# Kernel tuning notes

Hardware: AMD Instinct MI355X
Metric: run time of the kernel (lower is better)

## Reference

```python
import jax, jax.numpy as jnp
import numpy as np

LN_EPS = 1e-5

def _layernorm(x, g, b):
    mu = jnp.mean(x, axis=-1, keepdims=True)
    var = jnp.var(x, axis=-1, keepdims=True)
    return (x - mu) * jax.lax.rsqrt(var + LN_EPS) * g + b

def setup_inputs() -> dict:
    key = jax.random.key(0)
    B, S, D, H = 2, 2048, 1024, 16
    dh = D // H          # 64
    r = 48               # r_attn = int(0.75*min(D,dh))
    r_out = 768          # int(0.75*D)
    I = 4 * D            # GPT-2 MLP inner dim
    r_mlp = 512          # int(0.5*min(D,I))
    ks = jax.random.split(key, 24)
    sc = lambda *sh: 0.02
    inp = {
        'hidden_states': jax.random.normal(ks[0], (B, S, D), jnp.float32),
        'ln1_g': jnp.ones((D,), jnp.float32), 'ln1_b': jnp.zeros((D,), jnp.float32),
        'ln2_g': jnp.ones((D,), jnp.float32), 'ln2_b': jnp.zeros((D,), jnp.float32),
        'q_U': jax.random.normal(ks[1], (D, H, r), jnp.float32) * 0.02,
        'q_V': jax.random.normal(ks[2], (H, r, dh), jnp.float32) * 0.02,
        'q_b': jax.random.normal(ks[3], (H, dh), jnp.float32) * 0.02,
        'k_U': jax.random.normal(ks[4], (D, H, r), jnp.float32) * 0.02,
        'k_V': jax.random.normal(ks[5], (H, r, dh), jnp.float32) * 0.02,
        'k_b': jax.random.normal(ks[6], (H, dh), jnp.float32) * 0.02,
        'v_U': jax.random.normal(ks[7], (D, H, r), jnp.float32) * 0.02,
        'v_V': jax.random.normal(ks[8], (H, r, dh), jnp.float32) * 0.02,
        'v_b': jax.random.normal(ks[9], (H, dh), jnp.float32) * 0.02,
        'out_U': jax.random.normal(ks[10], (D, r_out), jnp.float32) * 0.02,
        'out_V': jax.random.normal(ks[11], (r_out, D), jnp.float32) * 0.02,
        'out_b': jnp.zeros((D,), jnp.float32),
        'fc1_U': jax.random.normal(ks[12], (D, r_mlp), jnp.float32) * 0.02,
        'fc1_V': jax.random.normal(ks[13], (r_mlp, I), jnp.float32) * 0.02,
        'fc1_b': jnp.zeros((I,), jnp.float32),
        'fc2_U': jax.random.normal(ks[14], (I, r_mlp), jnp.float32) * 0.02,
        'fc2_V': jax.random.normal(ks[15], (r_mlp, D), jnp.float32) * 0.02,
        'fc2_b': jnp.zeros((D,), jnp.float32),
    }
    return inp

def reference(hidden_states, ln1_g, ln1_b, ln2_g, ln2_b,
              q_U, q_V, q_b, k_U, k_V, k_b, v_U, v_V, v_b,
              out_U, out_V, out_b, fc1_U, fc1_V, fc1_b, fc2_U, fc2_V, fc2_b):
    B, S, D = hidden_states.shape
    H, dh = q_V.shape[0], q_V.shape[2]
    x = _layernorm(hidden_states, ln1_g, ln1_b)
    # low-rank per-head projections (latent P then reconstruct)
    Q = jnp.einsum('bsd,dhr,hre->bhse', x, q_U, q_V) + q_b[None, :, None, :]
    Pk = jnp.einsum('bsd,dhr->bhsr', x, k_U)
    Pv = jnp.einsum('bsd,dhr->bhsr', x, v_U)
    K = jnp.einsum('bhsr,hrd->bhsd', Pk, k_V) + k_b[None, :, None, :]
    V = jnp.einsum('bhsr,hrd->bhsd', Pv, v_V) + v_b[None, :, None, :]
    # causal scaled dot-product attention
    scale = 1.0 / jnp.sqrt(jnp.asarray(dh, x.dtype))
    scores = jnp.einsum('bhse,bhte->bhst', Q, K) * scale
    causal = jnp.tril(jnp.ones((S, S), bool))
    scores = jnp.where(causal[None, None], scores, jnp.asarray(-1e9, scores.dtype))
    attn = jax.nn.softmax(scores, axis=-1)
    ctx = jnp.einsum('bhst,bhtd->bhsd', attn, V)          # [B,H,S,dh]
    ctx = ctx.transpose(0, 2, 1, 3).reshape(B, S, D)
    attn_out = (ctx @ out_U) @ out_V + out_b
    h = hidden_states + attn_out
    # low-rank MLP with GPT-2 gelu (tanh approx)
    x2 = _layernorm(h, ln2_g, ln2_b)
    hmid = jax.nn.gelu((x2 @ fc1_U) @ fc1_V + fc1_b, approximate=True)
    mlp_out = (hmid @ fc2_U) @ fc2_V + fc2_b
    return h + mlp_out
```

## Files before the change

kernel.cpp:

```cpp
#include <hip/hip_runtime.h>
#include <hip/hip_bf16.h>

typedef float f32x4 __attribute__((ext_vector_type(4)));
typedef __bf16 bf16x8 __attribute__((ext_vector_type(8)));
typedef __bf16 bf16x4 __attribute__((ext_vector_type(4)));
typedef unsigned short u16x8 __attribute__((ext_vector_type(8)));
typedef unsigned short u16x4 __attribute__((ext_vector_type(4)));

#define QSCALE 0.180336881f

__device__ __forceinline__ unsigned short f2bf(float f) {
  union { float f; unsigned int u; } v; v.f = f;
  return (unsigned short)((v.u + 0x7FFFu + ((v.u >> 16) & 1u)) >> 16);
}

__device__ __forceinline__ f32x4 mfma16(bf16x8 a, bf16x8 b, f32x4 c) {
  return __builtin_amdgcn_mfma_f32_16x16x32_bf16(a, b, c, 0, 0, 0);
}

__device__ __forceinline__ void gload16(const unsigned short* g, unsigned short* l) {
  __builtin_amdgcn_global_load_lds(
      (const __attribute__((address_space(1))) void*)g,
      (__attribute__((address_space(3))) void*)l, 16, 0, 0);
}


__global__ void concat_bias_k(const float* __restrict__ qb, const float* __restrict__ kb,
                              const float* __restrict__ vb, float* __restrict__ out) {
  const int i = blockIdx.x * 256 + threadIdx.x;
  if (i >= 3072) return;
  const float* s = (i < 1024) ? qb : (i < 2048 ? kb : vb);
  out[i] = s[i & 1023] * (i < 1024 ? QSCALE : 1.0f);
}

__global__ void tcvt_k(const float* __restrict__ in, unsigned short* __restrict__ out,
                       int R, int C) {
  __shared__ float tile[32][33];
  const int x = blockIdx.x * 32 + threadIdx.x;
  const int y0 = blockIdx.y * 32;
#pragma unroll
  for (int i = 0; i < 32; i += 8)
    tile[threadIdx.y + i][threadIdx.x] = in[(size_t)(y0 + threadIdx.y + i) * C + x];
  __syncthreads();
  const int ox = y0 + threadIdx.x;
  const int oy0 = blockIdx.x * 32;
#pragma unroll
  for (int i = 0; i < 32; i += 8)
    out[(size_t)(oy0 + threadIdx.y + i) * R + ox] = f2bf(tile[threadIdx.x][threadIdx.y + i]);
}

__global__ void cvt_k(const float* __restrict__ in, unsigned short* __restrict__ out, int n) {
  const int i = (blockIdx.x * 256 + threadIdx.x) * 4;
  if (i >= n) return;
  const f32x4 v = *(const f32x4*)(in + i);
  u16x4 o;
#pragma unroll
  for (int k = 0; k < 4; ++k) o[k] = f2bf(v[k]);
  *(u16x4*)(out + i) = o;
}

__global__ void vtr_k(const unsigned short* __restrict__ QKV, unsigned short* __restrict__ VT) {
  __shared__ unsigned short tile[32][33];
  const int bh = blockIdx.z, b = bh >> 4, h = bh & 15;
  const int s0 = blockIdx.x * 32, d0 = blockIdx.y * 32;
  const unsigned short* src = QKV + (size_t)b * 2048 * 3072 + 2048 + h * 64;
#pragma unroll
  for (int i = 0; i < 32; i += 8)
    tile[threadIdx.y + i][threadIdx.x] = src[(size_t)(s0 + threadIdx.y + i) * 3072 + d0 + threadIdx.x];
  __syncthreads();
  unsigned short* dst = VT + (size_t)bh * 64 * 2048;
#pragma unroll
  for (int i = 0; i < 32; i += 8)
    dst[(size_t)(d0 + threadIdx.y + i) * 2048 + s0 + threadIdx.x] = tile[threadIdx.x][threadIdx.y + i];
}

__global__ __launch_bounds__(256) void wqkv_pre_k(
    const float* __restrict__ qU, const float* __restrict__ qV,
    const float* __restrict__ kU, const float* __restrict__ kV,
    const float* __restrict__ vU, const float* __restrict__ vV,
    unsigned short* __restrict__ WT) {
  __shared__ float Us[64][48];
  __shared__ float Vs[48][64];
  const int m = blockIdx.y >> 4, h = blockIdx.y & 15;
  const int d0 = blockIdx.x * 64;
  const float* U = (m == 0) ? qU : (m == 1 ? kU : vU);
  const float* V = (m == 0) ? qV : (m == 1 ? kV : vV);
  const float qs = (m == 0) ? QSCALE : 1.0f;
  const int t = threadIdx.x;
  for (int idx = t; idx < 64 * 48; idx += 256) {
    const int d = idx / 48, r = idx - d * 48;
    Us[d][r] = U[(size_t)(d0 + d) * 768 + h * 48 + r];
  }
  for (int idx = t; idx < 48 * 64; idx += 256) {
    const int r = idx >> 6, e = idx & 63;
    Vs[r][e] = V[(h * 48 + r) * 64 + e];
  }
  __syncthreads();
  const int e = t & 63, dg = t >> 6;
  for (int j = 0; j < 16; ++j) {
    const int d = dg * 16 + j;
    float s = 0.f;
#pragma unroll
    for (int r = 0; r < 48; ++r) s = fmaf(Us[d][r], Vs[r][e], s);
    WT[(size_t)(m * 1024 + h * 64 + e) * 1024 + d0 + d] = f2bf(s * qs);
  }
}

__global__ __launch_bounds__(256) void ln_k(
    const float* __restrict__ in, const float* __restrict__ gw,
    const float* __restrict__ bw, unsigned short* __restrict__ out) {
  const int row = blockIdx.x, t = threadIdx.x;
  const f32x4 v = *(const f32x4*)(in + (size_t)row * 1024 + t * 4);
  float s = v[0] + v[1] + v[2] + v[3];
  float ss = v[0] * v[0] + v[1] * v[1] + v[2] * v[2] + v[3] * v[3];
#pragma unroll
  for (int off = 1; off < 64; off <<= 1) {
    s += __shfl_xor(s, off);
    ss += __shfl_xor(ss, off);
  }
  __shared__ float red[8];
  if ((t & 63) == 0) { red[(t >> 6) * 2] = s; red[(t >> 6) * 2 + 1] = ss; }
  __syncthreads();
  s = red[0] + red[2] + red[4] + red[6];
  ss = red[1] + red[3] + red[5] + red[7];
  const float mean = s * (1.0f / 1024.0f);
  const float rstd = rsqrtf(ss * (1.0f / 1024.0f) - mean * mean + 1e-5f);
  const f32x4 g4 = *(const f32x4*)(gw + t * 4);
  const f32x4 b4 = *(const f32x4*)(bw + t * 4);
  u16x4 o;
#pragma unroll
  for (int i = 0; i < 4; ++i) o[i] = f2bf((v[i] - mean) * rstd * g4[i] + b4[i]);
  *(u16x4*)(out + (size_t)row * 1024 + t * 4) = o;
}

__device__ __forceinline__ void xcd_swz(int& bx, int& by, int nx, int ny) {
  const int nwg = nx * ny;
  if ((nwg & 7) == 0) {
    const int d = by * nx + bx;
    const int k = (d & 7) * (nwg >> 3) + (d >> 3);
    bx = k % nx;
    by = k / nx;
  }
}

template <int BM, int BN, int EPI, int OUTBF>
__global__ __launch_bounds__(256) void gemm_k(
    const unsigned short* __restrict__ A, const unsigned short* __restrict__ Bt,
    const float* __restrict__ bias, const float* __restrict__ resid,
    void* __restrict__ Cout, int M, int N, int K) {
  constexpr int MI = BM / 32;
  constexpr int FN = BN / 32;
  constexpr int NL = (BM == 128 ? 2 : 1) + (BN == 128 ? 2 : 1);
  constexpr int SM_KLOOP = 4 * (BM + BN) * 32;
  constexpr int SM_EPI = OUTBF ? 4 * (BM / 2) * 72 : 0;
  constexpr int SME = SM_KLOOP > SM_EPI ? SM_KLOOP : SM_EPI;
  __shared__ unsigned short smem[SME];
  unsigned short* As = smem;
  unsigned short* Bs = smem + 4 * BM * 32;
  int bxi = blockIdx.x, byi = blockIdx.y;
  xcd_swz(bxi, byi, gridDim.x, gridDim.y);
  const int t = threadIdx.x;
  const int lane = t & 63, wid = t >> 6;
  const int m0 = byi * BM, n0 = bxi * BN;
  const int wm = (wid >> 1) * (BM / 2), wn = (wid & 1) * (BN / 2);
  const int fr = lane & 15, fg = (lane >> 4) * 8;

  f32x4 acc[MI][FN];
#pragma unroll
  for (int i = 0; i < MI; ++i)
#pragma unroll
    for (int j = 0; j < FN; ++j) acc[i][j] = (f32x4){0.f, 0.f, 0.f, 0.f};

  const unsigned short* Ag0 = A + (size_t)(m0 + (t >> 2)) * K + (t & 3) * 8;
  const unsigned short* Ag1 = A + (size_t)(m0 + 64 + (t >> 2)) * K + (t & 3) * 8;
  const unsigned short* Bg0 = Bt + (size_t)(n0 + (t >> 2)) * K + (t & 3) * 8;
  const unsigned short* Bg1 = Bt + (size_t)(n0 + 64 + (t >> 2)) * K + (t & 3) * 8;
  const int l0 = t * 8;

#define GEMM_STAGE(buf, ke)                                             \
  {                                                                     \
    gload16(Ag0 + (ke), &As[(buf) * BM * 32 + l0]);                     \
    if (BM == 128) gload16(Ag1 + (ke), &As[(buf) * BM * 32 + l0 + 2048]); \
    gload16(Bg0 + (ke), &Bs[(buf) * BN * 32 + l0]);                     \
    if (BN == 128) gload16(Bg1 + (ke), &Bs[(buf) * BN * 32 + l0 + 2048]); \
  }

  const int nk = K >> 5;
  GEMM_STAGE(0, 0);
  if (nk > 1) GEMM_STAGE(1, 32);
  if (nk > 2) GEMM_STAGE(2, 64);

  for (int kt = 0; kt < nk; ++kt) {
    const int cur = kt & 3;
    if (kt + 2 < nk)
      asm volatile("s_waitcnt vmcnt(%0)" ::"n"(2 * NL) : "memory");
    else if (kt + 1 < nk)
      asm volatile("s_waitcnt vmcnt(%0)" ::"n"(NL) : "memory");
    else
      asm volatile("s_waitcnt vmcnt(0)" ::: "memory");
    __builtin_amdgcn_s_barrier();
    __builtin_amdgcn_sched_barrier(0);
    if (kt + 3 < nk) GEMM_STAGE((kt + 3) & 3, (kt + 3) * 32);
    bf16x8 af[MI], bfr[FN];
#pragma unroll
    for (int i = 0; i < MI; ++i)
      af[i] = *(const bf16x8*)&As[cur * BM * 32 + (wm + i * 16 + fr) * 32 + fg];
#pragma unroll
    for (int j = 0; j < FN; ++j)
      bfr[j] = *(const bf16x8*)&Bs[cur * BN * 32 + (wn + j * 16 + fr) * 32 + fg];
#pragma unroll
    for (int i = 0; i < MI; ++i)
#pragma unroll
      for (int j = 0; j < FN; ++j) acc[i][j] = mfma16(af[i], bfr[j], acc[i][j]);
  }
#undef GEMM_STAGE

  if (OUTBF) {
    __syncthreads();
    unsigned short* eb = smem + wid * ((BM / 2) * 72);
#pragma unroll
    for (int j = 0; j < FN; ++j) {
      const int colL = j * 16 + fr;
      const float bval = (EPI >= 1) ? bias[n0 + wn + colL] : 0.0f;
#pragma unroll
      for (int i = 0; i < MI; ++i) {
#pragma unroll
        for (int r = 0; r < 4; ++r) {
          const int rl = i * 16 + ((lane >> 4) << 2) + r;
          float v = acc[i][j][r] + bval;
          if (EPI == 2) {
            const float z = 0.7978845608028654f * (v + 0.044715f * v * v * v);
            v = v - v / (__expf(2.0f * z) + 1.0f);
          }
          eb[rl * 72 + colL] = f2bf(v);
        }
      }
    }
    __builtin_amdgcn_s_barrier();
    constexpr int CH = (BN / 2) / 8;
    constexpr int RPI = 64 / CH;
    const int c2 = lane % CH, r2b = lane / CH;
    unsigned short* Cg = (unsigned short*)Cout;
#pragma unroll
    for (int it = 0; it < (BM / 2) / RPI; ++it) {
      const int r2 = r2b + it * RPI;
      const u16x8 vv = *(const u16x8*)&eb[r2 * 72 + c2 * 8];
      *(u16x8*)&Cg[(size_t)(m0 + wm + r2) * N + n0 + wn + c2 * 8] = vv;
    }
  } else {
#pragma unroll
    for (int j = 0; j < FN; ++j) {
      const int col = n0 + wn + j * 16 + fr;
      const float bval = (EPI >= 1) ? bias[col] : 0.0f;
#pragma unroll
      for (int i = 0; i < MI; ++i) {
#pragma unroll
        for (int r = 0; r < 4; ++r) {
          const int row = m0 + wm + i * 16 + ((lane >> 4) << 2) + r;
          float v = acc[i][j][r] + bval;
          if (EPI == 3) v += resid[(size_t)row * N + col];
          ((float*)Cout)[(size_t)row * N + col] = v;
        }
      }
    }
  }
}

__global__ __launch_bounds__(512) void attn_k(
    const unsigned short* __restrict__ QKV, const unsigned short* __restrict__ VT,
    unsigned short* __restrict__ ctx) {
  __shared__ unsigned short Ks[2][64 * 64];
  __shared__ unsigned short Vs[2][64 * 64];
  __shared__ unsigned short Ps[8][16 * 64];
  int bxi = blockIdx.x, byi = blockIdx.y;
  xcd_swz(bxi, byi, 16, 32);
  const int qi = ((byi >> 1) & 1) ? (15 - bxi) : bxi;
  const int bh = byi, b = bh >> 4, h = bh & 15;
  const int nt = 2 * qi + 2;
  const int q0b = qi * 128;
  const int t = threadIdx.x, lane = t & 63, w = t >> 6;
  const int g = lane >> 4, c = lane & 15;
  const int cks = c & 7;
  const size_t base = (size_t)b * 2048 * 3072;

  const int r0 = t >> 3, ch0 = t & 7;
  const int lw = r0 * 64 + ((ch0 ^ (r0 & 7)) * 8);
  const unsigned short* Kg = QKV + base + 1024 + h * 64 + (size_t)r0 * 3072 + ch0 * 8;
  const unsigned short* Vg = VT + ((size_t)bh * 64 + r0) * 2048 + ch0 * 8;

  const int kro0 = (g ^ cks) * 8, kro1 = ((4 + g) ^ cks) * 8;

  bf16x8 onef;
#pragma unroll
  for (int i = 0; i < 8; ++i) onef[i] = (__bf16)1.0f;

  const int qrow = q0b + w * 16 + c;
  const unsigned short* qp = QKV + base + (size_t)qrow * 3072 + h * 64 + g * 8;
  const bf16x8 qf0 = *(const bf16x8*)qp;
  const bf16x8 qf1 = *(const bf16x8*)(qp + 32);

  f32x4 o[4];
#pragma unroll
  for (int d = 0; d < 4; ++d) o[d] = (f32x4){0.f, 0.f, 0.f, 0.f};
  f32x4 ol = (f32x4){0.f, 0.f, 0.f, 0.f};
  float mrow = -1e30f;

  u16x8 kr, vr;
#define ATTN_LOAD(kt_)                                        \
  {                                                           \
    kr = *(const u16x8*)(Kg + (size_t)(kt_) * 64 * 3072);     \
    vr = *(const u16x8*)(Vg + (kt_) * 64);                    \
  }
#define ATTN_WRITE(buf)                                       \
  {                                                           \
    *(u16x8*)&Ks[buf][lw] = kr;                               \
    *(u16x8*)&Vs[buf][lw] = vr;                               \
  }

  ATTN_LOAD(0);
  ATTN_WRITE(0);
  if (nt > 1) ATTN_LOAD(1);
  __syncthreads();

  const int fsrc = g * 20;

  for (int j = 0; j < nt; ++j) {
    const int cur = j & 1;
    const int kbase = j * 64;
    const bool active = (kbase <= q0b + w * 16 + 15);

    if (active) {
      f32x4 s4[4];
      __builtin_amdgcn_s_setprio(1);
#pragma unroll
      for (int t16 = 0; t16 < 4; ++t16) {
        const int krow = (t16 * 16 + c) * 64;
        const bf16x8 kf0 = *(const bf16x8*)&Ks[cur][krow + kro0];
        const bf16x8 kf1 = *(const bf16x8*)&Ks[cur][krow + kro1];
        f32x4 a = (f32x4){0.f, 0.f, 0.f, 0.f};
        a = mfma16(kf0, qf0, a);
        a = mfma16(kf1, qf1, a);
        s4[t16] = a;
      }
      __builtin_amdgcn_s_setprio(0);
      if (kbase + 63 > qrow) {
#pragma unroll
        for (int t16 = 0; t16 < 4; ++t16)
#pragma unroll
          for (int r = 0; r < 4; ++r)
            if (kbase + t16 * 16 + 4 * g + r > qrow) s4[t16][r] = -1e30f;
      }
      float mx = s4[0][0];
#pragma unroll
      for (int t16 = 0; t16 < 4; ++t16)
#pragma unroll
        for (int r = 0; r < 4; ++r) mx = fmaxf(mx, s4[t16][r]);
      mx = fmaxf(mx, __shfl_xor(mx, 16));
      mx = fmaxf(mx, __shfl_xor(mx, 32));
      if (!__all(mx <= mrow + 8.0f)) {
        const float mn = fmaxf(mrow, mx);
        const float fac = exp2f(mrow - mn);
        mrow = mn;
        float fo[4];
#pragma unroll
        for (int r = 0; r < 4; ++r) fo[r] = __shfl(fac, fsrc + r);
#pragma unroll
        for (int d = 0; d < 4; ++d)
#pragma unroll
          for (int r = 0; r < 4; ++r) o[d][r] *= fo[r];
#pragma unroll
        for (int r = 0; r < 4; ++r) ol[r] *= fo[r];
      }
#pragma unroll
      for (int t16 = 0; t16 < 4; ++t16) {
        bf16x4 pw;
#pragma unroll
        for (int r = 0; r < 4; ++r) pw[r] = (__bf16)exp2f(s4[t16][r] - mrow);
        *(bf16x4*)&Ps[w][c * 64 + (((2 * t16 + (g >> 1)) ^ cks) * 8) + (g & 1) * 4] = pw;
      }
      __builtin_amdgcn_s_setprio(1);
#pragma unroll
      for (int ks = 0; ks < 2; ++ks) {
        const int po = ((ks * 4 + g) ^ cks) * 8;
        const bf16x8 pf = *(const bf16x8*)&Ps[w][c * 64 + po];
#pragma unroll
        for (int d = 0; d < 4; ++d) {
          const bf16x8 vf = *(const bf16x8*)&Vs[cur][(d * 16 + c) * 64 + po];
          o[d] = mfma16(pf, vf, o[d]);
        }
        ol = mfma16(pf, onef, ol);
      }
      __builtin_amdgcn_s_setprio(0);
    }

    if (j + 1 < nt) {
      __syncthreads();
      ATTN_WRITE(cur ^ 1);
      if (j + 2 < nt) ATTN_LOAD(j + 2);
      __syncthreads();
    }
  }
#pragma unroll
  for (int d = 0; d < 4; ++d)
#pragma unroll
    for (int r = 0; r < 4; ++r) {
      const float v = o[d][r] / ol[r];
      ctx[(size_t)(b * 2048 + q0b + w * 16 + g * 4 + r) * 1024 + h * 64 + d * 16 + c] = f2bf(v);
    }
#undef ATTN_LOAD
#undef ATTN_WRITE
}


extern "C" void kernel_launch(void* const* d_in, const int* in_sizes, int n_in,
                              void* d_out, int out_size, void* d_ws, size_t ws_size,
                              hipStream_t stream) {
  const float* hidden = (const float*)d_in[0];
  const float* ln1g = (const float*)d_in[1];
  const float* ln1b = (const float*)d_in[2];
  const float* ln2g = (const float*)d_in[3];
  const float* ln2b = (const float*)d_in[4];
  const float* qU = (const float*)d_in[5];
  const float* qV = (const float*)d_in[6];
  const float* qb = (const float*)d_in[7];
  const float* kU = (const float*)d_in[8];
  const float* kV = (const float*)d_in[9];
  const float* kb = (const float*)d_in[10];
  const float* vU = (const float*)d_in[11];
  const float* vV = (const float*)d_in[12];
  const float* vb = (const float*)d_in[13];
  const float* outU = (const float*)d_in[14];
  const float* outV = (const float*)d_in[15];
  const float* outb = (const float*)d_in[16];
  const float* fc1U = (const float*)d_in[17];
  const float* fc1V = (const float*)d_in[18];
  const float* fc1b = (const float*)d_in[19];
  const float* fc2U = (const float*)d_in[20];
  const float* fc2V = (const float*)d_in[21];
  const float* fc2b = (const float*)d_in[22];
  float* out = (float*)d_out;

  char* p = (char*)d_ws;
  unsigned short* x1x2 = (unsigned short*)p; p += (size_t)4096 * 1024 * 2;
  unsigned short* WqT_t1 = (unsigned short*)p; p += (size_t)3072 * 1024 * 2;
  float* bqkv = (float*)p; p += 3072 * 4;
  char* bigA = p; p += (size_t)4096 * 3072 * 2 + (size_t)4096 * 1024 * 2;
  unsigned short* QKV = (unsigned short*)bigA;
  unsigned short* ctxb = (unsigned short*)(bigA + (size_t)4096 * 3072 * 2);
  unsigned short* hmid = (unsigned short*)bigA;
  char* wo = p; p += (size_t)1024 * 768 * 2 * 2 + (size_t)1024 * 1024 * 2;
  unsigned short* outUb = (unsigned short*)wo;
  unsigned short* outVT = (unsigned short*)(wo + (size_t)1024 * 768 * 2);
  unsigned short* WoutT = (unsigned short*)(wo + (size_t)1024 * 768 * 2 * 2);
  unsigned short* t2 = (unsigned short*)wo;
  float* hbuf = (float*)p; p += (size_t)4096 * 1024 * 4;
  unsigned short* VT = (unsigned short*)hbuf;
  unsigned short* fc1UT = (unsigned short*)p; p += (size_t)512 * 1024 * 2;
  unsigned short* fc1VT = (unsigned short*)p; p += (size_t)4096 * 512 * 2;
  unsigned short* fc2UT = (unsigned short*)p; p += (size_t)512 * 4096 * 2;
  unsigned short* fc2VT = (unsigned short*)p; p += (size_t)1024 * 512 * 2;

  const dim3 b256(256);
  const dim3 tb(32, 8);

  concat_bias_k<<<12, b256, 0, stream>>>(qb, kb, vb, bqkv);
  wqkv_pre_k<<<dim3(16, 48), b256, 0, stream>>>(qU, qV, kU, kV, vU, vV, WqT_t1);
  tcvt_k<<<dim3(32, 24), tb, 0, stream>>>(outV, outVT, 768, 1024);
  cvt_k<<<768, b256, 0, stream>>>(outU, outUb, 1024 * 768);
  tcvt_k<<<dim3(16, 32), tb, 0, stream>>>(fc1U, fc1UT, 1024, 512);
  tcvt_k<<<dim3(128, 16), tb, 0, stream>>>(fc1V, fc1VT, 512, 4096);
  tcvt_k<<<dim3(16, 128), tb, 0, stream>>>(fc2U, fc2UT, 4096, 512);
  tcvt_k<<<dim3(32, 16), tb, 0, stream>>>(fc2V, fc2VT, 512, 1024);

  ln_k<<<4096, b256, 0, stream>>>(hidden, ln1g, ln1b, x1x2);
  gemm_k<128, 128, 1, 1><<<dim3(24, 32), b256, 0, stream>>>(x1x2, WqT_t1, bqkv, nullptr, QKV, 4096, 3072, 1024);
  vtr_k<<<dim3(64, 2, 32), tb, 0, stream>>>(QKV, VT);
  gemm_k<128, 128, 0, 1><<<dim3(8, 8), b256, 0, stream>>>(outVT, outUb, nullptr, nullptr, WoutT, 1024, 1024, 768);
  attn_k<<<dim3(16, 32), dim3(512), 0, stream>>>(QKV, VT, ctxb);
  gemm_k<64, 128, 3, 0><<<dim3(8, 64), b256, 0, stream>>>(ctxb, WoutT, outb, hidden, hbuf, 4096, 1024, 1024);

  ln_k<<<4096, b256, 0, stream>>>(hbuf, ln2g, ln2b, x1x2);
  gemm_k<64, 64, 0, 1><<<dim3(8, 64), b256, 0, stream>>>(x1x2, fc1UT, nullptr, nullptr, WqT_t1, 4096, 512, 1024);
  gemm_k<128, 128, 2, 1><<<dim3(32, 32), b256, 0, stream>>>(WqT_t1, fc1VT, fc1b, nullptr, hmid, 4096, 4096, 512);
  gemm_k<64, 64, 0, 1><<<dim3(8, 64), b256, 0, stream>>>(hmid, fc2UT, nullptr, nullptr, t2, 4096, 512, 4096);
  gemm_k<64, 128, 3, 0><<<dim3(8, 64), b256, 0, stream>>>(t2, fc2VT, fc2b, hbuf, out, 4096, 1024, 512);
}
```

Measured before the change: 266.7 us.

## Add 256x256 eight-wave GEMM kernel for QKV and fc1 projections

Adds a 256x256 tile GEMM with 512 threads, triple-buffered LDS staging, and global loads interleaved between MFMA groups under raised wave priority. It replaces the 128x128 kernel for the QKV projection and the fc1 expansion with GELU. Larger tiles raise data reuse per LDS byte and cut global traffic. The cost is fewer workgroups (192 and 256 on a 256-CU part, so partial occupancy for QKV) and heavy register and LDS pressure.

New measurement: 259.1 us. 2.9% less time.

```diff
diff --git a/kernel.cpp b/kernel.cpp
--- a/kernel.cpp
+++ b/kernel.cpp
@@ -143,6 +143,130 @@
   }
 }
 
+#define WVM(N) asm volatile("s_waitcnt vmcnt(%0)" ::"n"(N) : "memory")
+
+template <int EPI>
+__global__ __launch_bounds__(512) void gemm256_k(
+    const unsigned short* __restrict__ A, const unsigned short* __restrict__ Bt,
+    const float* __restrict__ bias, unsigned short* __restrict__ Cout,
+    int M, int N, int K) {
+  __shared__ unsigned short smem[49152];
+  unsigned short* Asm = smem;
+  unsigned short* Bsm = smem + 24576;
+  int bxi = blockIdx.x, byi = blockIdx.y;
+  xcd_swz(bxi, byi, gridDim.x, gridDim.y);
+  const int t = threadIdx.x;
+  const int lane = t & 63, wid = t >> 6;
+  const int wr = wid >> 2, wc = wid & 3;
+  const int m0 = byi * 256, n0 = bxi * 256;
+  const int fr = lane & 15, g = lane >> 4;
+
+  f32x4 acc[8][4];
+#pragma unroll
+  for (int i = 0; i < 8; ++i)
+#pragma unroll
+    for (int j = 0; j < 4; ++j) acc[i][j] = (f32x4){0.f, 0.f, 0.f, 0.f};
+
+  const unsigned short* Ag0 = A + (size_t)(m0 + (t >> 2)) * K + (t & 3) * 8;
+  const unsigned short* Ag1 = A + (size_t)(m0 + 128 + (t >> 2)) * K + (t & 3) * 8;
+  const unsigned short* Bg0 = Bt + (size_t)(n0 + (t >> 2)) * K + (t & 3) * 8;
+  const unsigned short* Bg1 = Bt + (size_t)(n0 + 128 + (t >> 2)) * K + (t & 3) * 8;
+  const int l8 = t * 8;
+
+#define SA0(BUF, KT) gload16(Ag0 + (KT) * 32, &Asm[(BUF) * 8192 + l8]);
+#define SA1(BUF, KT) gload16(Ag1 + (KT) * 32, &Asm[(BUF) * 8192 + 4096 + l8]);
+#define SB0(BUF, KT) gload16(Bg0 + (KT) * 32, &Bsm[(BUF) * 8192 + l8]);
+#define SB1(BUF, KT) gload16(Bg1 + (KT) * 32, &Bsm[(BUF) * 8192 + 4096 + l8]);
+
+  const int nk = K >> 5;
+  SA0(0, 0) SA1(0, 0) SB0(0, 0) SB1(0, 0)
+  SA0(1, 1) SA1(1, 1) SB0(1, 1) SB1(1, 1)
+
+  int buf = 0, nbuf = 2;
+  for (int kt = 0; kt < nk; ++kt) {
+    if (kt + 1 < nk) WVM(4); else WVM(0);
+    __builtin_amdgcn_s_barrier();
+    const unsigned short* Aw = &Asm[buf * 8192 + wr * 4096];
+    const unsigned short* Bw = &Bsm[buf * 8192 + (wc >> 1) * 4096 + (wc & 1) * 2048];
+    const bool st = (kt + 2 < nk);
+    const int kf = kt + 2;
+    bf16x8 af[4], af2[4], bf[4];
+#pragma unroll
+    for (int i = 0; i < 4; ++i) af[i] = *(const bf16x8*)&Aw[(i * 16 + fr) * 32 + g * 8];
+#pragma unroll
+    for (int j = 0; j < 2; ++j) bf[j] = *(const bf16x8*)&Bw[(j * 16 + fr) * 32 + g * 8];
+    if (st) SA0(nbuf, kf)
+    __builtin_amdgcn_s_setprio(1);
+#pragma unroll
+    for (int i = 0; i < 4; ++i)
+#pragma unroll
+      for (int j = 0; j < 2; ++j) acc[i][j] = mfma16(af[i], bf[j], acc[i][j]);
+    __builtin_amdgcn_s_setprio(0);
+#pragma unroll
+    for (int j = 2; j < 4; ++j) bf[j] = *(const bf16x8*)&Bw[(j * 16 + fr) * 32 + g * 8];
+    if (st) SA1(nbuf, kf)
+    __builtin_amdgcn_s_setprio(1);
+#pragma unroll
+    for (int i = 0; i < 4; ++i)
+#pragma unroll
+      for (int j = 2; j < 4; ++j) acc[i][j] = mfma16(af[i], bf[j], acc[i][j]);
+    __builtin_amdgcn_s_setprio(0);
+#pragma unroll
+    for (int i = 0; i < 4; ++i) af2[i] = *(const bf16x8*)&Aw[(64 + i * 16 + fr) * 32 + g * 8];
+    if (st) SB0(nbuf, kf)
+    __builtin_amdgcn_s_setprio(1);
+#pragma unroll
+    for (int i = 0; i < 4; ++i)
+#pragma unroll
+      for (int j = 0; j < 2; ++j) acc[4 + i][j] = mfma16(af2[i], bf[j], acc[4 + i][j]);
+    __builtin_amdgcn_s_setprio(0);
+    if (st) SB1(nbuf, kf)
+    __builtin_amdgcn_s_setprio(1);
+#pragma unroll
+    for (int i = 0; i < 4; ++i)
+#pragma unroll
+      for (int j = 2; j < 4; ++j) acc[4 + i][j] = mfma16(af2[i], bf[j], acc[4 + i][j]);
+    __builtin_amdgcn_s_setprio(0);
+    buf = (buf == 2) ? 0 : buf + 1;
+    nbuf = (nbuf == 2) ? 0 : nbuf + 1;
+  }
+#undef SA0
+#undef SA1
+#undef SB0
+#undef SB1
+
+  __syncthreads();
+  unsigned short* eb = smem + wid * 4608;
+#pragma unroll
+  for (int ih = 0; ih < 2; ++ih) {
+#pragma unroll
+    for (int j = 0; j < 4; ++j) {
+      const int colL = j * 16 + fr;
+      const float bval = bias[n0 + wc * 64 + colL];
+#pragma unroll
+      for (int i2 = 0; i2 < 4; ++i2) {
+#pragma unroll
+        for (int r = 0; r < 4; ++r) {
+          const int rl = i2 * 16 + g * 4 + r;
+          float v = acc[ih * 4 + i2][j][r] + bval;
+          if (EPI == 2) {
+            const float z = 0.7978845608028654f * (v + 0.044715f * v * v * v);
+            v = v - v / (__expf(2.0f * z) + 1.0f);
+          }
+          eb[rl * 72 + colL] = f2bf(v);
+        }
+      }
+    }
+#pragma unroll
+    for (int it = 0; it < 8; ++it) {
+      const int row = (lane >> 3) + it * 8;
+      const int ch = lane & 7;
+      const u16x8 vv = *(const u16x8*)&eb[row * 72 + ch * 8];
+      *(u16x8*)&Cout[(size_t)(m0 + wr * 128 + ih * 64 + row) * N + n0 + wc * 64 + ch * 8] = vv;
+    }
+  }
+}
+
 template <int BM, int BN, int EPI, int OUTBF>
 __global__ __launch_bounds__(256) void gemm_k(
     const unsigned short* __restrict__ A, const unsigned short* __restrict__ Bt,
@@ -151,12 +275,13 @@
   constexpr int MI = BM / 32;
   constexpr int FN = BN / 32;
   constexpr int NL = (BM == 128 ? 2 : 1) + (BN == 128 ? 2 : 1);
-  constexpr int SM_KLOOP = 4 * (BM + BN) * 32;
+  constexpr int ASZ = BM * 32, BSZ = BN * 32;
+  constexpr int SM_KLOOP = 4 * (ASZ + BSZ);
   constexpr int SM_EPI = OUTBF ? 4 * (BM / 2) * 72 : 0;
   constexpr int SME = SM_KLOOP > SM_EPI ? SM_KLOOP : SM_EPI;
   __shared__ unsigned short smem[SME];
   unsigned short* As = smem;
-  unsigned short* Bs = smem + 4 * BM * 32;
+  unsigned short* Bs = smem + 4 * ASZ;
   int bxi = blockIdx.x, byi = blockIdx.y;
   xcd_swz(bxi, byi, gridDim.x, gridDim.y);
   const int t = threadIdx.x;
@@ -177,12 +302,12 @@
   const unsigned short* Bg1 = Bt + (size_t)(n0 + 64 + (t >> 2)) * K + (t & 3) * 8;
   const int l0 = t * 8;
 
-#define GEMM_STAGE(buf, ke)                                             \
-  {                                                                     \
-    gload16(Ag0 + (ke), &As[(buf) * BM * 32 + l0]);                     \
-    if (BM == 128) gload16(Ag1 + (ke), &As[(buf) * BM * 32 + l0 + 2048]); \
-    gload16(Bg0 + (ke), &Bs[(buf) * BN * 32 + l0]);                     \
-    if (BN == 128) gload16(Bg1 + (ke), &Bs[(buf) * BN * 32 + l0 + 2048]); \
+#define GEMM_STAGE(buf, ke)                                               \
+  {                                                                       \
+    gload16(Ag0 + (ke), &As[(buf) * ASZ + l0]);                           \
+    if (BM == 128) gload16(Ag1 + (ke), &As[(buf) * ASZ + l0 + 2048]);     \
+    gload16(Bg0 + (ke), &Bs[(buf) * BSZ + l0]);                           \
+    if (BN == 128) gload16(Bg1 + (ke), &Bs[(buf) * BSZ + l0 + 2048]);     \
   }
 
   const int nk = K >> 5;
@@ -193,21 +318,21 @@
   for (int kt = 0; kt < nk; ++kt) {
     const int cur = kt & 3;
     if (kt + 2 < nk)
-      asm volatile("s_waitcnt vmcnt(%0)" ::"n"(2 * NL) : "memory");
+      WVM(2 * NL);
     else if (kt + 1 < nk)
-      asm volatile("s_waitcnt vmcnt(%0)" ::"n"(NL) : "memory");
+      WVM(NL);
     else
-      asm volatile("s_waitcnt vmcnt(0)" ::: "memory");
+      WVM(0);
     __builtin_amdgcn_s_barrier();
     __builtin_amdgcn_sched_barrier(0);
     if (kt + 3 < nk) GEMM_STAGE((kt + 3) & 3, (kt + 3) * 32);
     bf16x8 af[MI], bfr[FN];
 #pragma unroll
     for (int i = 0; i < MI; ++i)
-      af[i] = *(const bf16x8*)&As[cur * BM * 32 + (wm + i * 16 + fr) * 32 + fg];
+      af[i] = *(const bf16x8*)&As[cur * ASZ + (wm + i * 16 + fr) * 32 + fg];
 #pragma unroll
     for (int j = 0; j < FN; ++j)
-      bfr[j] = *(const bf16x8*)&Bs[cur * BN * 32 + (wn + j * 16 + fr) * 32 + fg];
+      bfr[j] = *(const bf16x8*)&Bs[cur * BSZ + (wn + j * 16 + fr) * 32 + fg];
 #pragma unroll
     for (int i = 0; i < MI; ++i)
 #pragma unroll
@@ -473,7 +598,7 @@
   tcvt_k<<<dim3(32, 16), tb, 0, stream>>>(fc2V, fc2VT, 512, 1024);
 
   ln_k<<<4096, b256, 0, stream>>>(hidden, ln1g, ln1b, x1x2);
-  gemm_k<128, 128, 1, 1><<<dim3(24, 32), b256, 0, stream>>>(x1x2, WqT_t1, bqkv, nullptr, QKV, 4096, 3072, 1024);
+  gemm256_k<1><<<dim3(12, 16), dim3(512), 0, stream>>>(x1x2, WqT_t1, bqkv, QKV, 4096, 3072, 1024);
   vtr_k<<<dim3(64, 2, 32), tb, 0, stream>>>(QKV, VT);
   gemm_k<128, 128, 0, 1><<<dim3(8, 8), b256, 0, stream>>>(outVT, outUb, nullptr, nullptr, WoutT, 1024, 1024, 768);
   attn_k<<<dim3(16, 32), dim3(512), 0, stream>>>(QKV, VT, ctxb);
@@ -481,7 +606,7 @@
 
   ln_k<<<4096, b256, 0, stream>>>(hbuf, ln2g, ln2b, x1x2);
   gemm_k<64, 64, 0, 1><<<dim3(8, 64), b256, 0, stream>>>(x1x2, fc1UT, nullptr, nullptr, WqT_t1, 4096, 512, 1024);
-  gemm_k<128, 128, 2, 1><<<dim3(32, 32), b256, 0, stream>>>(WqT_t1, fc1VT, fc1b, nullptr, hmid, 4096, 4096, 512);
+  gemm256_k<2><<<dim3(16, 16), dim3(512), 0, stream>>>(WqT_t1, fc1VT, fc1b, hmid, 4096, 4096, 512);
   gemm_k<64, 64, 0, 1><<<dim3(8, 64), b256, 0, stream>>>(hmid, fc2UT, nullptr, nullptr, t2, 4096, 512, 4096);
   gemm_k<64, 128, 3, 0><<<dim3(8, 64), b256, 0, stream>>>(t2, fc2VT, fc2b, hbuf, out, 4096, 1024, 512);
 }
```

## Shrink GEMM LDS to double buffer, chunk epilogue, use smaller N tiles

Applied to the files above, without the earlier changes.

The GEMM pipeline goes from four LDS stages (three loads in flight, explicit vmcnt waits) to a plain two-stage double buffer with __syncthreads. The bf16 epilogue is staged through a fixed 32-row LDS slab in two passes, so its LDS footprint no longer grows with BM. Several launches switch to 64-wide N tiles with more blocks. Together these cut LDS per block and raise block count and occupancy, at the cost of shallower prefetch and less reuse per tile.

After: 288.3 us. 1.08x slower.

```diff
diff --git a/kernel.cpp b/kernel.cpp
--- a/kernel.cpp
+++ b/kernel.cpp
@@ -150,13 +150,13 @@
     void* __restrict__ Cout, int M, int N, int K) {
   constexpr int MI = BM / 32;
   constexpr int FN = BN / 32;
-  constexpr int NL = (BM == 128 ? 2 : 1) + (BN == 128 ? 2 : 1);
-  constexpr int SM_KLOOP = 4 * (BM + BN) * 32;
-  constexpr int SM_EPI = OUTBF ? 4 * (BM / 2) * 72 : 0;
+  constexpr int ASZ = BM * 32, BSZ = BN * 32;
+  constexpr int SM_KLOOP = 2 * (ASZ + BSZ);
+  constexpr int SM_EPI = OUTBF ? 4 * 32 * 72 : 0;
   constexpr int SME = SM_KLOOP > SM_EPI ? SM_KLOOP : SM_EPI;
   __shared__ unsigned short smem[SME];
   unsigned short* As = smem;
-  unsigned short* Bs = smem + 4 * BM * 32;
+  unsigned short* Bs = smem + 2 * ASZ;
   int bxi = blockIdx.x, byi = blockIdx.y;
   xcd_swz(bxi, byi, gridDim.x, gridDim.y);
   const int t = threadIdx.x;
@@ -177,37 +177,28 @@
   const unsigned short* Bg1 = Bt + (size_t)(n0 + 64 + (t >> 2)) * K + (t & 3) * 8;
   const int l0 = t * 8;
 
-#define GEMM_STAGE(buf, ke)                                             \
-  {                                                                     \
-    gload16(Ag0 + (ke), &As[(buf) * BM * 32 + l0]);                     \
-    if (BM == 128) gload16(Ag1 + (ke), &As[(buf) * BM * 32 + l0 + 2048]); \
-    gload16(Bg0 + (ke), &Bs[(buf) * BN * 32 + l0]);                     \
-    if (BN == 128) gload16(Bg1 + (ke), &Bs[(buf) * BN * 32 + l0 + 2048]); \
+#define GEMM_STAGE(buf, ke)                                               \
+  {                                                                       \
+    gload16(Ag0 + (ke), &As[(buf) * ASZ + l0]);                           \
+    if (BM == 128) gload16(Ag1 + (ke), &As[(buf) * ASZ + l0 + 2048]);     \
+    gload16(Bg0 + (ke), &Bs[(buf) * BSZ + l0]);                           \
+    if (BN == 128) gload16(Bg1 + (ke), &Bs[(buf) * BSZ + l0 + 2048]);     \
   }
 
   const int nk = K >> 5;
   GEMM_STAGE(0, 0);
-  if (nk > 1) GEMM_STAGE(1, 32);
-  if (nk > 2) GEMM_STAGE(2, 64);
 
   for (int kt = 0; kt < nk; ++kt) {
-    const int cur = kt & 3;
-    if (kt + 2 < nk)
-      asm volatile("s_waitcnt vmcnt(%0)" ::"n"(2 * NL) : "memory");
-    else if (kt + 1 < nk)
-      asm volatile("s_waitcnt vmcnt(%0)" ::"n"(NL) : "memory");
-    else
-      asm volatile("s_waitcnt vmcnt(0)" ::: "memory");
-    __builtin_amdgcn_s_barrier();
-    __builtin_amdgcn_sched_barrier(0);
-    if (kt + 3 < nk) GEMM_STAGE((kt + 3) & 3, (kt + 3) * 32);
+    const int cur = kt & 1;
+    __syncthreads();
+    if (kt + 1 < nk) GEMM_STAGE(cur ^ 1, (kt + 1) * 32);
     bf16x8 af[MI], bfr[FN];
 #pragma unroll
     for (int i = 0; i < MI; ++i)
-      af[i] = *(const bf16x8*)&As[cur * BM * 32 + (wm + i * 16 + fr) * 32 + fg];
+      af[i] = *(const bf16x8*)&As[cur * ASZ + (wm + i * 16 + fr) * 32 + fg];
 #pragma unroll
     for (int j = 0; j < FN; ++j)
-      bfr[j] = *(const bf16x8*)&Bs[cur * BN * 32 + (wn + j * 16 + fr) * 32 + fg];
+      bfr[j] = *(const bf16x8*)&Bs[cur * BSZ + (wn + j * 16 + fr) * 32 + fg];
 #pragma unroll
     for (int i = 0; i < MI; ++i)
 #pragma unroll
@@ -217,35 +208,37 @@
 
   if (OUTBF) {
     __syncthreads();
-    unsigned short* eb = smem + wid * ((BM / 2) * 72);
-#pragma unroll
-    for (int j = 0; j < FN; ++j) {
-      const int colL = j * 16 + fr;
-      const float bval = (EPI >= 1) ? bias[n0 + wn + colL] : 0.0f;
-#pragma unroll
-      for (int i = 0; i < MI; ++i) {
-#pragma unroll
-        for (int r = 0; r < 4; ++r) {
-          const int rl = i * 16 + ((lane >> 4) << 2) + r;
-          float v = acc[i][j][r] + bval;
-          if (EPI == 2) {
-            const float z = 0.7978845608028654f * (v + 0.044715f * v * v * v);
-            v = v - v / (__expf(2.0f * z) + 1.0f);
+    unsigned short* eb = smem + wid * (32 * 72);
+    unsigned short* Cg = (unsigned short*)Cout;
+    constexpr int CH = (BN / 2) / 8;
+    constexpr int RPS = 64 / CH;
+    const int c2 = lane % CH, r2b = lane / CH;
+#pragma unroll
+    for (int hp = 0; hp < MI / 2; ++hp) {
+#pragma unroll
+      for (int j = 0; j < FN; ++j) {
+        const int colL = j * 16 + fr;
+        const float bval = (EPI >= 1) ? bias[n0 + wn + colL] : 0.0f;
+#pragma unroll
+        for (int i2 = 0; i2 < 2; ++i2) {
+#pragma unroll
+          for (int r = 0; r < 4; ++r) {
+            const int rl = i2 * 16 + ((lane >> 4) << 2) + r;
+            float v = acc[hp * 2 + i2][j][r] + bval;
+            if (EPI == 2) {
+              const float z = 0.7978845608028654f * (v + 0.044715f * v * v * v);
+              v = v - v / (__expf(2.0f * z) + 1.0f);
+            }
+            eb[rl * 72 + colL] = f2bf(v);
           }
-          eb[rl * 72 + colL] = f2bf(v);
         }
       }
-    }
-    __builtin_amdgcn_s_barrier();
-    constexpr int CH = (BN / 2) / 8;
-    constexpr int RPI = 64 / CH;
-    const int c2 = lane % CH, r2b = lane / CH;
-    unsigned short* Cg = (unsigned short*)Cout;
-#pragma unroll
-    for (int it = 0; it < (BM / 2) / RPI; ++it) {
-      const int r2 = r2b + it * RPI;
-      const u16x8 vv = *(const u16x8*)&eb[r2 * 72 + c2 * 8];
-      *(u16x8*)&Cg[(size_t)(m0 + wm + r2) * N + n0 + wn + c2 * 8] = vv;
+#pragma unroll
+      for (int it = 0; it < 32 / RPS; ++it) {
+        const int r2 = r2b + it * RPS;
+        const u16x8 vv = *(const u16x8*)&eb[r2 * 72 + c2 * 8];
+        *(u16x8*)&Cg[(size_t)(m0 + wm + hp * 32 + r2) * N + n0 + wn + c2 * 8] = vv;
+      }
     }
   } else {
 #pragma unroll
@@ -473,15 +466,15 @@
   tcvt_k<<<dim3(32, 16), tb, 0, stream>>>(fc2V, fc2VT, 512, 1024);
 
   ln_k<<<4096, b256, 0, stream>>>(hidden, ln1g, ln1b, x1x2);
-  gemm_k<128, 128, 1, 1><<<dim3(24, 32), b256, 0, stream>>>(x1x2, WqT_t1, bqkv, nullptr, QKV, 4096, 3072, 1024);
+  gemm_k<128, 64, 1, 1><<<dim3(48, 32), b256, 0, stream>>>(x1x2, WqT_t1, bqkv, nullptr, QKV, 4096, 3072, 1024);
   vtr_k<<<dim3(64, 2, 32), tb, 0, stream>>>(QKV, VT);
   gemm_k<128, 128, 0, 1><<<dim3(8, 8), b256, 0, stream>>>(outVT, outUb, nullptr, nullptr, WoutT, 1024, 1024, 768);
   attn_k<<<dim3(16, 32), dim3(512), 0, stream>>>(QKV, VT, ctxb);
-  gemm_k<64, 128, 3, 0><<<dim3(8, 64), b256, 0, stream>>>(ctxb, WoutT, outb, hidden, hbuf, 4096, 1024, 1024);
+  gemm_k<64, 64, 3, 0><<<dim3(16, 64), b256, 0, stream>>>(ctxb, WoutT, outb, hidden, hbuf, 4096, 1024, 1024);
 
   ln_k<<<4096, b256, 0, stream>>>(hbuf, ln2g, ln2b, x1x2);
   gemm_k<64, 64, 0, 1><<<dim3(8, 64), b256, 0, stream>>>(x1x2, fc1UT, nullptr, nullptr, WqT_t1, 4096, 512, 1024);
-  gemm_k<128, 128, 2, 1><<<dim3(32, 32), b256, 0, stream>>>(WqT_t1, fc1VT, fc1b, nullptr, hmid, 4096, 4096, 512);
+  gemm_k<128, 64, 2, 1><<<dim3(64, 32), b256, 0, stream>>>(WqT_t1, fc1VT, fc1b, nullptr, hmid, 4096, 4096, 512);
   gemm_k<64, 64, 0, 1><<<dim3(8, 64), b256, 0, stream>>>(hmid, fc2UT, nullptr, nullptr, t2, 4096, 512, 4096);
-  gemm_k<64, 128, 3, 0><<<dim3(8, 64), b256, 0, stream>>>(t2, fc2VT, fc2b, hbuf, out, 4096, 1024, 512);
-}
+  gemm_k<64, 64, 3, 0><<<dim3(16, 64), b256, 0, stream>>>(t2, fc2VT, fc2b, hbuf, out, 4096, 1024, 512);
+}
```
